# Kernel tuning notes

Measured on AMD Instinct MI355X. Metric: run time of the kernel, lower is better.

## Reference

```python
import jax, jax.numpy as jnp
import numpy as np

N_NODES = 50000
N_EDGES = 500000
F_DIM = 128
N_REL = 8
N_LAYERS = 2
NEG_SLOPE = 0.2  # PyG RGATConv default negative_slope


def setup_inputs() -> dict:
    key = jax.random.key(0)
    ks = jax.random.split(key, 6)
    x = jax.random.normal(ks[0], (N_NODES, F_DIM), dtype=jnp.float32)
    edge_index = jax.random.randint(ks[1], (2, N_EDGES), 0, N_NODES)
    edge_type = jax.random.randint(ks[2], (N_EDGES,), 0, N_REL)
    # Per-layer relation weights [L, R, F_in, F_out], attention vectors q,k [L, F_out, 1], bias [L, F_out]
    W = jax.random.normal(ks[3], (N_LAYERS, N_REL, F_DIM, F_DIM), dtype=jnp.float32) * (1.0 / np.sqrt(F_DIM)).astype(np.float32)
    att_q = jax.random.normal(ks[4], (N_LAYERS, F_DIM, 1), dtype=jnp.float32) * 0.1
    att_k = jax.random.normal(ks[5], (N_LAYERS, F_DIM, 1), dtype=jnp.float32) * 0.1
    bias = jnp.zeros((N_LAYERS, F_DIM), dtype=jnp.float32)
    return {"x": x, "W": W, "att_q": att_q, "att_k": att_k, "bias": bias,
            "edge_index": edge_index, "edge_type": edge_type}


def _segment_softmax(logits, seg, num_segments):
    # Numerically stable softmax over edges grouped by destination node.
    m = jax.ops.segment_max(logits, seg, num_segments=num_segments)
    m = jax.lax.stop_gradient(m)
    e = jnp.exp(logits - m[seg])
    denom = jax.ops.segment_sum(e, seg, num_segments=num_segments)
    return e / (denom[seg] + 1e-16)


def _rgat_layer(h, src, dst, edge_type, W, q, k, b):
    # h: [N, F]; W: [R, F, F]. Project once per relation, then gather per edge
    # (avoids materializing [E, F, F] per-edge weight gathers).
    n = h.shape[0]
    xw = jnp.einsum('nf,rfg->rng', h, W)          # [R, N, F]
    out_j = xw[edge_type, src]                    # [E, F] transformed source feats
    out_i = xw[edge_type, dst]                    # [E, F] transformed dest feats
    # additive self-attention: leaky_relu(q(x_i) + k(x_j)), heads=1, dim=1
    logits = jax.nn.leaky_relu((out_i @ q + out_j @ k)[:, 0], NEG_SLOPE)  # [E]
    alpha = _segment_softmax(logits, dst, n)      # across-relation softmax per dst node
    agg = jax.ops.segment_sum(alpha[:, None] * out_j, dst, num_segments=n)  # [N, F]
    return agg + b


def reference(x, W, att_q, att_k, bias, edge_index, edge_type):
    src, dst = edge_index[0], edge_index[1]
    h = x
    for l in range(W.shape[0]):  # small fixed layer count
        h = _rgat_layer(h, src, dst, edge_type, W[l], att_q[l], att_k[l], bias[l])
        h = jax.nn.relu(h)  # dropout is identity in eval mode
    return h
```

## Files before the change

kernel.cpp:

```cpp
#include <hip/hip_runtime.h>
#include <hip/hip_bf16.h>
#include <hip/hip_fp16.h>

#define N_NODES 50000
#define N_EDGES 500000
#define F_DIM   128
#define N_REL   8
#define N_LAYERS 2
#define NEG_SLOPE 0.2f

#define NBLK_N ((N_NODES + 255) / 256)

typedef _Float16 half8 __attribute__((ext_vector_type(8)));
typedef float f32x4  __attribute__((ext_vector_type(4)));


__device__ inline float lrelu(float l) { return (l > 0.f) ? l : NEG_SLOPE * l; }

__global__ __launch_bounds__(256) void prep_h(const float* __restrict__ H,
                                              _Float16* __restrict__ Hf) {
    const size_t i8 = (size_t)blockIdx.x * 256 + threadIdx.x;
    if (i8 >= (size_t)N_NODES * F_DIM / 8) return;
    const float* src = H + i8 * 8;
    float av[8];
    *(float4*)(av)     = *(const float4*)(src);
    *(float4*)(av + 4) = *(const float4*)(src + 4);
    alignas(16) _Float16 hb[8];
#pragma unroll
    for (int j = 0; j < 8; ++j) hb[j] = (_Float16)av[j];
    *(uint4*)(Hf + i8 * 8) = *(const uint4*)hb;
}

__global__ __launch_bounds__(256) void prep_w(const float* __restrict__ W,
                                              _Float16* __restrict__ Wf) {
    __shared__ float tile[64][F_DIM + 1];
    const int mat = blockIdx.x;
    const float* src = W + (size_t)mat * F_DIM * F_DIM;
    const int t = threadIdx.x;
    for (int hf = 0; hf < 2; ++hf) {
#pragma unroll
        for (int i = 0; i < 8; ++i) {
            int idx = t + i * 256;
            int f = idx >> 5, c4 = idx & 31;
            float4 v = *(const float4*)(src + (size_t)(hf * 64 + f) * F_DIM + c4 * 4);
            *(float4*)&tile[f][c4 * 4] = v;
        }
        __syncthreads();
        int g = t >> 1, fs = (t & 1) * 32;
        for (int c = 0; c < 4; ++c) {
            alignas(16) _Float16 th[8];
#pragma unroll
            for (int j = 0; j < 8; ++j) th[j] = (_Float16)tile[fs + c * 8 + j][g];
            size_t o = ((size_t)mat * F_DIM + g) * F_DIM + hf * 64 + fs + c * 8;
            *(uint4*)(Wf + o) = *(const uint4*)th;
        }
        __syncthreads();
    }
}

#define GBM 128
__global__ __launch_bounds__(256, 2) void gemm_xw(const _Float16* __restrict__ Hf,
                                                  const _Float16* __restrict__ Wf,
                                                  const float* __restrict__ qv_g,
                                                  const float* __restrict__ kv_g,
                                                  __half* __restrict__ xw,
                                                  float* __restrict__ a_q,
                                                  float* __restrict__ a_k) {
    __shared__ _Float16 lds[F_DIM * F_DIM];
    const int rb0 = blockIdx.x * GBM;
    const int r   = blockIdx.y;
    const int tid = threadIdx.x;
    const int lane = tid & 63, w = tid >> 6;
    const int q = lane >> 4, ln = lane & 15;

    {
        const _Float16* src = Wf + (size_t)r * F_DIM * F_DIM;
#pragma unroll
        for (int i = 0; i < 8; ++i) {
            int chunk = tid + i * 256;
            int gg = chunk >> 4, c8 = chunk & 15;
            uint4 v = *(const uint4*)(src + gg * F_DIM + c8 * 8);
            *(uint4*)(lds + gg * F_DIM + ((c8 ^ (gg & 15)) * 8)) = v;
        }
    }

    half8 Af[2][4];
#pragma unroll
    for (int rt = 0; rt < 2; ++rt) {
        int row = rb0 + w * 32 + rt * 16 + ln;
        int ar = (row < N_NODES) ? row : (N_NODES - 1);
        const _Float16* hp = Hf + (size_t)ar * F_DIM;
#pragma unroll
        for (int ks = 0; ks < 4; ++ks)
            Af[rt][ks] = *(const half8*)(hp + ks * 32 + q * 8);
    }

    float qvl[8], kvl[8];
#pragma unroll
    for (int t = 0; t < 8; ++t) {
        qvl[t] = qv_g[t * 16 + ln];
        kvl[t] = kv_g[t * 16 + ln];
    }

    __syncthreads();

    f32x4 acc[2][8];
#pragma unroll
    for (int rt = 0; rt < 2; ++rt)
#pragma unroll
        for (int t = 0; t < 8; ++t) acc[rt][t] = (f32x4)(0.f);

#pragma unroll
    for (int ks = 0; ks < 4; ++ks) {
        const int jx = (((ks * 4 + q) ^ ln)) << 3;
        half8 Bf[8];
#pragma unroll
        for (int c = 0; c < 8; ++c)
            Bf[c] = *(const half8*)(lds + (c * 16 + ln) * F_DIM + jx);
#pragma unroll
        for (int c = 0; c < 8; ++c)
#pragma unroll
            for (int rt = 0; rt < 2; ++rt)
                acc[rt][c] = __builtin_amdgcn_mfma_f32_16x16x32_f16(Af[rt][ks], Bf[c], acc[rt][c], 0, 0, 0);
    }

#pragma unroll
    for (int rt = 0; rt < 2; ++rt) {
        float pq[4], pk[4];
#pragma unroll
        for (int reg = 0; reg < 4; ++reg) {
            const int row = rb0 + w * 32 + rt * 16 + q * 4 + reg;
            alignas(16) unsigned short hs[8];
            float sq = 0.f, sk = 0.f;
#pragma unroll
            for (int t = 0; t < 8; ++t) {
                float v = acc[rt][t][reg];
                __half hv = __float2half(v);
                hs[t] = *reinterpret_cast<unsigned short*>(&hv);
                sq = fmaf(v, qvl[t], sq);
                sk = fmaf(v, kvl[t], sk);
            }
            if (row < N_NODES)
                *(uint4*)(xw + ((size_t)r * N_NODES + row) * F_DIM + ln * 8) = *(const uint4*)hs;
            pq[reg] = sq; pk[reg] = sk;
        }
#pragma unroll
        for (int reg = 0; reg < 4; ++reg) {
#pragma unroll
            for (int m = 1; m <= 8; m <<= 1) {
                pq[reg] += __shfl_xor(pq[reg], m);
                pk[reg] += __shfl_xor(pk[reg], m);
            }
        }
        if (ln == 0) {
#pragma unroll
            for (int reg = 0; reg < 4; ++reg) {
                const int row = rb0 + w * 32 + rt * 16 + q * 4 + reg;
                if (row < N_NODES) {
                    a_q[r * N_NODES + row] = pq[reg];
                    a_k[r * N_NODES + row] = pk[reg];
                }
            }
        }
    }
}


__global__ __launch_bounds__(256) void count_kernel(const int* __restrict__ dstp,
                                                    int* __restrict__ cnt) {
    int e = blockIdx.x * 256 + threadIdx.x;
    if (e < N_EDGES) atomicAdd(cnt + dstp[e], 1);
}

__global__ __launch_bounds__(256) void block_sum_kernel(const int* __restrict__ cnt,
                                                        int* __restrict__ partial) {
    __shared__ int s[256];
    int idx = blockIdx.x * 256 + threadIdx.x;
    int v = (idx < N_NODES) ? cnt[idx] : 0;
    s[threadIdx.x] = v;
    __syncthreads();
    for (int off = 128; off > 0; off >>= 1) {
        if (threadIdx.x < off) s[threadIdx.x] += s[threadIdx.x + off];
        __syncthreads();
    }
    if (threadIdx.x == 0) partial[blockIdx.x] = s[0];
}

__global__ __launch_bounds__(256) void scan_partials_kernel(int* __restrict__ partial,
                                                            int* __restrict__ row_ptr) {
    __shared__ int s[256];
    int t = threadIdx.x;
    int v = (t < NBLK_N) ? partial[t] : 0;
    s[t] = v;
    __syncthreads();
#pragma unroll
    for (int off = 1; off < 256; off <<= 1) {
        int x = (t >= off) ? s[t - off] : 0;
        __syncthreads();
        s[t] += x;
        __syncthreads();
    }
    if (t < NBLK_N) partial[t] = s[t] - v;
    if (t == 0) row_ptr[N_NODES] = N_EDGES;
}

__global__ __launch_bounds__(256) void scan_block_kernel(const int* __restrict__ cnt,
                                                         const int* __restrict__ partial,
                                                         int* __restrict__ row_ptr) {
    __shared__ int s[256];
    int t = threadIdx.x;
    int idx = blockIdx.x * 256 + t;
    int v = (idx < N_NODES) ? cnt[idx] : 0;
    s[t] = v;
    __syncthreads();
#pragma unroll
    for (int off = 1; off < 256; off <<= 1) {
        int x = (t >= off) ? s[t - off] : 0;
        __syncthreads();
        s[t] += x;
        __syncthreads();
    }
    if (idx < N_NODES) row_ptr[idx] = partial[blockIdx.x] + s[t] - v;
}

__global__ __launch_bounds__(256) void scatter_kernel(const int* __restrict__ srcp,
                                                      const int* __restrict__ dstp,
                                                      const int* __restrict__ etp,
                                                      const int* __restrict__ row_ptr,
                                                      int* __restrict__ cursor,
                                                      unsigned* __restrict__ sorted,
                                                      unsigned short* __restrict__ dst16) {
    int e = blockIdx.x * 256 + threadIdx.x;
    if (e >= N_EDGES) return;
    int d = dstp[e];
    int pos = atomicAdd(cursor + d, 1);
    int j = row_ptr[d] + pos;
    sorted[j] = (unsigned)srcp[e] | ((unsigned)etp[e] << 16);
    dst16[j] = (unsigned short)d;
}

__global__ __launch_bounds__(256) void logits_kernel(const float* __restrict__ a_q,
                                                     const float* __restrict__ a_k,
                                                     const unsigned* __restrict__ sorted,
                                                     const unsigned short* __restrict__ dst16,
                                                     float* __restrict__ lgt) {
    int j = blockIdx.x * 256 + threadIdx.x;
    if (j >= N_EDGES) return;
    unsigned p = sorted[j];
    int s = p & 0xffff, t = p >> 16;
    int d = dst16[j];
    lgt[j] = lrelu(a_q[t * N_NODES + d] + a_k[t * N_NODES + s]);
}

__device__ inline void accum8(float* acc, uint4 v, float a) {
    const __half2* h2 = reinterpret_cast<const __half2*>(&v);
#pragma unroll
    for (int t = 0; t < 4; ++t) {
        float2 f = __half22float2(h2[t]);
        acc[t * 2]     = fmaf(a, f.x, acc[t * 2]);
        acc[t * 2 + 1] = fmaf(a, f.y, acc[t * 2 + 1]);
    }
}
__device__ inline const uint4* xwrow(const __half* xw, unsigned p, int ln) {
    return (const uint4*)(xw + (((size_t)(p >> 16)) * N_NODES + (p & 0xffff)) * F_DIM + ln * 8);
}

__global__ __launch_bounds__(256) void agg_fused(const __half* __restrict__ xw,
                                                 const float* __restrict__ lgt,
                                                 const int* __restrict__ row_ptr,
                                                 const unsigned* __restrict__ sorted,
                                                 const float* __restrict__ bias,
                                                 float* __restrict__ outp,
                                                 _Float16* __restrict__ hfp) {
    const int lane = threadIdx.x & 63;
    const int wave = threadIdx.x >> 6;
    const int d = blockIdx.x * 4 + wave;
    if (d >= N_NODES) return;
    const int beg = row_ptr[d], end = row_ptr[d + 1];
    const int cnt = end - beg;
    const int g = lane >> 4, ln = lane & 15;

    if (cnt <= 64) {
        unsigned p = 0;
        float l = -3.4e38f;
        if (lane < cnt) {
            p = sorted[beg + lane];
            l = lgt[beg + lane];
        }
        float m = l;
#pragma unroll
        for (int off = 32; off > 0; off >>= 1) m = fmaxf(m, __shfl_xor(m, off));
        const float ex = (lane < cnt) ? __expf(l - m) : 0.f;

        float acc[8] = {0, 0, 0, 0, 0, 0, 0, 0};
        for (int i = 0; i < cnt; i += 8) {
            unsigned p0 = __shfl(p, i + g);
            unsigned p1 = __shfl(p, i + 4 + g);
            float a0 = __shfl(ex, i + g);
            float a1 = __shfl(ex, i + 4 + g);
            uint4 v0 = *xwrow(xw, p0, ln);
            uint4 v1 = *xwrow(xw, p1, ln);
            accum8(acc, v0, a0);
            accum8(acc, v1, a1);
        }
        float dsum = ex;
#pragma unroll
        for (int off = 32; off > 0; off >>= 1) dsum += __shfl_xor(dsum, off);
#pragma unroll
        for (int t = 0; t < 8; ++t) {
            acc[t] += __shfl_xor(acc[t], 16);
            acc[t] += __shfl_xor(acc[t], 32);
        }
        if (g == 0) {
            const float inv = 1.f / (dsum + 1e-16f);
#pragma unroll
            for (int t = 0; t < 8; ++t) {
                const int col = t * 16 + ln;
                const float v = fmaxf(fmaf(acc[t], inv, bias[col]), 0.f);
                if (outp) outp[(size_t)d * F_DIM + col] = v;
                if (hfp)  hfp[(size_t)d * F_DIM + col] = (_Float16)v;
            }
        }
    } else {
        const int p0 = lane * 2;
        const int c0 = (p0 & 7) * 16 + (p0 >> 3);
        const int c1 = c0 + 16;
        float2 acc = make_float2(bias[c0], bias[c1]);
        float m = -3.4e38f;
        for (int i = beg + lane; i < end; i += 64) m = fmaxf(m, lgt[i]);
#pragma unroll
        for (int off = 32; off > 0; off >>= 1) m = fmaxf(m, __shfl_xor(m, off));
        float dsum = 0.f;
        for (int i = beg + lane; i < end; i += 64) dsum += __expf(lgt[i] - m);
#pragma unroll
        for (int off = 32; off > 0; off >>= 1) dsum += __shfl_xor(dsum, off);
        const float inv = 1.f / (dsum + 1e-16f);
        for (int i = beg; i < end; ++i) {
            unsigned p = sorted[i];
            float alpha = __expf(lgt[i] - m) * inv;
            const __half2 h2 = *((const __half2*)xw + (((size_t)(p >> 16)) * N_NODES + (p & 0xffff)) * (F_DIM / 2) + lane);
            float2 v = make_float2(__half2float(h2.x), __half2float(h2.y));
            acc.x = fmaf(alpha, v.x, acc.x);
            acc.y = fmaf(alpha, v.y, acc.y);
        }
        const float v0 = fmaxf(acc.x, 0.f), v1 = fmaxf(acc.y, 0.f);
        if (outp) { outp[(size_t)d * F_DIM + c0] = v0; outp[(size_t)d * F_DIM + c1] = v1; }
        if (hfp)  { hfp[(size_t)d * F_DIM + c0] = (_Float16)v0; hfp[(size_t)d * F_DIM + c1] = (_Float16)v1; }
    }
}


extern "C" void kernel_launch(void* const* d_in, const int* in_sizes, int n_in,
                              void* d_out, int out_size, void* d_ws, size_t ws_size,
                              hipStream_t stream) {
    const float* x     = (const float*)d_in[0];
    const float* W     = (const float*)d_in[1];
    const float* att_q = (const float*)d_in[2];
    const float* att_k = (const float*)d_in[3];
    const float* bias  = (const float*)d_in[4];
    const int* ei      = (const int*)d_in[5];
    const int* etp     = (const int*)d_in[6];
    const int* srcp = ei;
    const int* dstp = ei + N_EDGES;
    float* out = (float*)d_out;
    char* ws   = (char*)d_ws;

    size_t off = 0;
    auto alloc = [&](size_t bytes) {
        void* p = ws + off;
        off = (off + bytes + 511) & ~(size_t)511;
        return p;
    };
    __half* xw       = (__half*)alloc((size_t)N_REL * N_NODES * F_DIM * sizeof(__half));
    float* a_q       = (float*)alloc((size_t)N_REL * N_NODES * sizeof(float));
    float* a_k       = (float*)alloc((size_t)N_REL * N_NODES * sizeof(float));
    int* cnt         = (int*)alloc((size_t)2 * N_NODES * sizeof(int));
    int* cursor      = cnt + N_NODES;
    int* row_ptr     = (int*)alloc(((size_t)N_NODES + 1) * sizeof(int));
    int* partial     = (int*)alloc(256 * sizeof(int));
    unsigned* sorted = (unsigned*)alloc((size_t)N_EDGES * sizeof(unsigned));
    unsigned short* dst16 = (unsigned short*)alloc((size_t)N_EDGES * sizeof(unsigned short));
    float* lgt       = (float*)alloc((size_t)N_EDGES * sizeof(float));
    _Float16* Wf     = (_Float16*)alloc((size_t)N_LAYERS * N_REL * F_DIM * F_DIM * sizeof(_Float16));
    _Float16* Hf     = (_Float16*)alloc((size_t)N_NODES * F_DIM * sizeof(_Float16));

    prep_w<<<N_LAYERS * N_REL, 256, 0, stream>>>(W, Wf);
    hipMemsetAsync(cnt, 0, (size_t)2 * N_NODES * 4, stream);
    count_kernel<<<(N_EDGES + 255) / 256, 256, 0, stream>>>(dstp, cnt);
    block_sum_kernel<<<NBLK_N, 256, 0, stream>>>(cnt, partial);
    scan_partials_kernel<<<1, 256, 0, stream>>>(partial, row_ptr);
    scan_block_kernel<<<NBLK_N, 256, 0, stream>>>(cnt, partial, row_ptr);
    scatter_kernel<<<(N_EDGES + 255) / 256, 256, 0, stream>>>(
        srcp, dstp, etp, row_ptr, cursor, sorted, dst16);

    const int grid_h = (N_NODES * F_DIM / 8 + 255) / 256;
    const int grid_m = (N_NODES + GBM - 1) / GBM;
    const int grid_e = (N_EDGES + 255) / 256;
    prep_h<<<grid_h, 256, 0, stream>>>(x, Hf);
    for (int l = 0; l < N_LAYERS; ++l) {
        gemm_xw<<<dim3(grid_m, N_REL), 256, 0, stream>>>(
            Hf, Wf + (size_t)l * N_REL * F_DIM * F_DIM,
            att_q + l * F_DIM, att_k + l * F_DIM,
            xw, a_q, a_k);
        logits_kernel<<<grid_e, 256, 0, stream>>>(a_q, a_k, sorted, dst16, lgt);
        const bool last = (l == N_LAYERS - 1);
        agg_fused<<<(N_NODES + 3) / 4, 256, 0, stream>>>(
            xw, lgt, row_ptr, sorted, bias + l * F_DIM,
            last ? out : nullptr,
            last ? nullptr : Hf);
    }
}
```

Baseline: 301.5 us.

## Aggregate raw features per relation then project, folding attention into W·q vectors

Instead of materializing the per-relation projection xw for all nodes (R×N×F fp16), the attention scalars are computed directly from H times precomputed W·q and W·k vectors. Edges are sorted by (dst, relation), raw source features are aggregated per relation, and then multiplied by W_r with MFMA inside the aggregation kernel. This removes the large xw write and read traffic and the dense R-fold GEMM, in exchange for a more complex aggregation kernel with per-relation synchronisation, extra CSR preprocessing, and fp16 rounding of aggregated sums.

Measured after the change: 571.1 us. +89.4%, slower.

```diff
diff --git a/kernel.cpp b/kernel.cpp
--- a/kernel.cpp
+++ b/kernel.cpp
@@ -16,6 +16,16 @@
 
 
 __device__ inline float lrelu(float l) { return (l > 0.f) ? l : NEG_SLOPE * l; }
+
+__device__ inline void accum8h(float* a, uint4 v, float al) {
+    const __half2* h2 = reinterpret_cast<const __half2*>(&v);
+#pragma unroll
+    for (int t = 0; t < 4; ++t) {
+        float2 f = __half22float2(h2[t]);
+        a[t * 2]     = fmaf(al, f.x, a[t * 2]);
+        a[t * 2 + 1] = fmaf(al, f.y, a[t * 2 + 1]);
+    }
+}
 
 __global__ __launch_bounds__(256) void prep_h(const float* __restrict__ H,
                                               _Float16* __restrict__ Hf) {
@@ -58,118 +68,67 @@
     }
 }
 
-#define GBM 128
-__global__ __launch_bounds__(256, 2) void gemm_xw(const _Float16* __restrict__ Hf,
-                                                  const _Float16* __restrict__ Wf,
-                                                  const float* __restrict__ qv_g,
-                                                  const float* __restrict__ kv_g,
-                                                  __half* __restrict__ xw,
+__global__ __launch_bounds__(256) void prep_vqk(const float* __restrict__ W,
+                                                const float* __restrict__ att_q,
+                                                const float* __restrict__ att_k,
+                                                _Float16* __restrict__ vb) {
+    const int l = blockIdx.x >> 3, r = blockIdx.x & 7;
+    __shared__ float qk[2 * F_DIM];
+    const int t = threadIdx.x;
+    qk[t] = (t < F_DIM) ? att_q[l * F_DIM + t] : att_k[l * F_DIM + (t - F_DIM)];
+    __syncthreads();
+    const float* Wr = W + ((size_t)(l * N_REL + r)) * F_DIM * F_DIM;
+    const int f = t & (F_DIM - 1);
+    const float* qv = (t < F_DIM) ? qk : qk + F_DIM;
+    float s = 0.f;
+    for (int g = 0; g < F_DIM; g += 4) {
+        float4 wv = *(const float4*)(Wr + (size_t)f * F_DIM + g);
+        s += wv.x * qv[g] + wv.y * qv[g + 1] + wv.z * qv[g + 2] + wv.w * qv[g + 3];
+    }
+    const int c = (t < F_DIM) ? r : (N_REL + r);
+    vb[((size_t)l * 16 + c) * F_DIM + f] = (_Float16)s;
+}
+
+__global__ __launch_bounds__(256) void aqk_kernel(const _Float16* __restrict__ Hf,
+                                                  const _Float16* __restrict__ vbl,
                                                   float* __restrict__ a_q,
                                                   float* __restrict__ a_k) {
-    __shared__ _Float16 lds[F_DIM * F_DIM];
-    const int rb0 = blockIdx.x * GBM;
-    const int r   = blockIdx.y;
-    const int tid = threadIdx.x;
-    const int lane = tid & 63, w = tid >> 6;
+    const int w = threadIdx.x >> 6, lane = threadIdx.x & 63;
     const int q = lane >> 4, ln = lane & 15;
-
-    {
-        const _Float16* src = Wf + (size_t)r * F_DIM * F_DIM;
-#pragma unroll
-        for (int i = 0; i < 8; ++i) {
-            int chunk = tid + i * 256;
-            int gg = chunk >> 4, c8 = chunk & 15;
-            uint4 v = *(const uint4*)(src + gg * F_DIM + c8 * 8);
-            *(uint4*)(lds + gg * F_DIM + ((c8 ^ (gg & 15)) * 8)) = v;
-        }
-    }
-
-    half8 Af[2][4];
-#pragma unroll
-    for (int rt = 0; rt < 2; ++rt) {
-        int row = rb0 + w * 32 + rt * 16 + ln;
-        int ar = (row < N_NODES) ? row : (N_NODES - 1);
-        const _Float16* hp = Hf + (size_t)ar * F_DIM;
-#pragma unroll
-        for (int ks = 0; ks < 4; ++ks)
-            Af[rt][ks] = *(const half8*)(hp + ks * 32 + q * 8);
-    }
-
-    float qvl[8], kvl[8];
-#pragma unroll
-    for (int t = 0; t < 8; ++t) {
-        qvl[t] = qv_g[t * 16 + ln];
-        kvl[t] = kv_g[t * 16 + ln];
-    }
-
-    __syncthreads();
-
-    f32x4 acc[2][8];
-#pragma unroll
-    for (int rt = 0; rt < 2; ++rt)
-#pragma unroll
-        for (int t = 0; t < 8; ++t) acc[rt][t] = (f32x4)(0.f);
-
+    const int row0 = blockIdx.x * 64 + w * 16;
+    f32x4 acc = (f32x4)(0.f);
 #pragma unroll
     for (int ks = 0; ks < 4; ++ks) {
-        const int jx = (((ks * 4 + q) ^ ln)) << 3;
-        half8 Bf[8];
-#pragma unroll
-        for (int c = 0; c < 8; ++c)
-            Bf[c] = *(const half8*)(lds + (c * 16 + ln) * F_DIM + jx);
-#pragma unroll
-        for (int c = 0; c < 8; ++c)
-#pragma unroll
-            for (int rt = 0; rt < 2; ++rt)
-                acc[rt][c] = __builtin_amdgcn_mfma_f32_16x16x32_f16(Af[rt][ks], Bf[c], acc[rt][c], 0, 0, 0);
-    }
-
-#pragma unroll
-    for (int rt = 0; rt < 2; ++rt) {
-        float pq[4], pk[4];
-#pragma unroll
-        for (int reg = 0; reg < 4; ++reg) {
-            const int row = rb0 + w * 32 + rt * 16 + q * 4 + reg;
-            alignas(16) unsigned short hs[8];
-            float sq = 0.f, sk = 0.f;
-#pragma unroll
-            for (int t = 0; t < 8; ++t) {
-                float v = acc[rt][t][reg];
-                __half hv = __float2half(v);
-                hs[t] = *reinterpret_cast<unsigned short*>(&hv);
-                sq = fmaf(v, qvl[t], sq);
-                sk = fmaf(v, kvl[t], sk);
-            }
-            if (row < N_NODES)
-                *(uint4*)(xw + ((size_t)r * N_NODES + row) * F_DIM + ln * 8) = *(const uint4*)hs;
-            pq[reg] = sq; pk[reg] = sk;
-        }
-#pragma unroll
-        for (int reg = 0; reg < 4; ++reg) {
-#pragma unroll
-            for (int m = 1; m <= 8; m <<= 1) {
-                pq[reg] += __shfl_xor(pq[reg], m);
-                pk[reg] += __shfl_xor(pk[reg], m);
-            }
-        }
-        if (ln == 0) {
-#pragma unroll
-            for (int reg = 0; reg < 4; ++reg) {
-                const int row = rb0 + w * 32 + rt * 16 + q * 4 + reg;
-                if (row < N_NODES) {
-                    a_q[r * N_NODES + row] = pq[reg];
-                    a_k[r * N_NODES + row] = pk[reg];
-                }
-            }
-        }
-    }
-}
-
-
-__global__ __launch_bounds__(256) void count_kernel(const int* __restrict__ dstp,
-                                                    int* __restrict__ cnt) {
+        int rr = row0 + ln; if (rr >= N_NODES) rr = N_NODES - 1;
+        half8 af = *(const half8*)(Hf + (size_t)rr * F_DIM + ks * 32 + q * 8);
+        half8 bf = *(const half8*)(vbl + (size_t)ln * F_DIM + ks * 32 + q * 8);
+        acc = __builtin_amdgcn_mfma_f32_16x16x32_f16(af, bf, acc, 0, 0, 0);
+    }
+#pragma unroll
+    for (int reg = 0; reg < 4; ++reg) {
+        const int row = row0 + q * 4 + reg;
+        if (row < N_NODES) {
+            if (ln < N_REL) a_q[ln * N_NODES + row] = acc[reg];
+            else            a_k[(ln - N_REL) * N_NODES + row] = acc[reg];
+        }
+    }
+}
+
+
+__global__ __launch_bounds__(256) void count2_kernel(const int* __restrict__ dstp,
+                                                     const int* __restrict__ etp,
+                                                     int* __restrict__ cnt2) {
     int e = blockIdx.x * 256 + threadIdx.x;
-    if (e < N_EDGES) atomicAdd(cnt + dstp[e], 1);
+    if (e < N_EDGES) atomicAdd(cnt2 + dstp[e] * N_REL + etp[e], 1);
+}
+
+__global__ __launch_bounds__(256) void sum8_kernel(const int* __restrict__ cnt2,
+                                                   int* __restrict__ cnt) {
+    int d = blockIdx.x * 256 + threadIdx.x;
+    if (d >= N_NODES) return;
+    int4 a = *(const int4*)(cnt2 + d * 8);
+    int4 b = *(const int4*)(cnt2 + d * 8 + 4);
+    cnt[d] = a.x + a.y + a.z + a.w + b.x + b.y + b.z + b.w;
 }
 
 __global__ __launch_bounds__(256) void block_sum_kernel(const int* __restrict__ cnt,
@@ -223,19 +182,35 @@
     if (idx < N_NODES) row_ptr[idx] = partial[blockIdx.x] + s[t] - v;
 }
 
-__global__ __launch_bounds__(256) void scatter_kernel(const int* __restrict__ srcp,
-                                                      const int* __restrict__ dstp,
-                                                      const int* __restrict__ etp,
-                                                      const int* __restrict__ row_ptr,
-                                                      int* __restrict__ cursor,
-                                                      unsigned* __restrict__ sorted,
-                                                      unsigned short* __restrict__ dst16) {
+__global__ __launch_bounds__(256) void rp2_kernel(const int* __restrict__ cnt2,
+                                                  const int* __restrict__ row_ptr,
+                                                  int* __restrict__ rp2) {
+    int d = blockIdx.x * 256 + threadIdx.x;
+    if (d == 0) rp2[(size_t)N_NODES * 8] = N_EDGES;
+    if (d >= N_NODES) return;
+    int4 a = *(const int4*)(cnt2 + d * 8);
+    int4 b = *(const int4*)(cnt2 + d * 8 + 4);
+    int rp = row_ptr[d];
+    int o[8];
+    o[0] = rp;          o[1] = o[0] + a.x;  o[2] = o[1] + a.y;  o[3] = o[2] + a.z;
+    o[4] = o[3] + a.w;  o[5] = o[4] + b.x;  o[6] = o[5] + b.y;  o[7] = o[6] + b.z;
+    *(int4*)(rp2 + d * 8)     = make_int4(o[0], o[1], o[2], o[3]);
+    *(int4*)(rp2 + d * 8 + 4) = make_int4(o[4], o[5], o[6], o[7]);
+}
+
+__global__ __launch_bounds__(256) void scatter2_kernel(const int* __restrict__ srcp,
+                                                       const int* __restrict__ dstp,
+                                                       const int* __restrict__ etp,
+                                                       const int* __restrict__ rp2,
+                                                       int* __restrict__ cursor2,
+                                                       unsigned* __restrict__ sorted,
+                                                       unsigned short* __restrict__ dst16) {
     int e = blockIdx.x * 256 + threadIdx.x;
     if (e >= N_EDGES) return;
-    int d = dstp[e];
-    int pos = atomicAdd(cursor + d, 1);
-    int j = row_ptr[d] + pos;
-    sorted[j] = (unsigned)srcp[e] | ((unsigned)etp[e] << 16);
+    int d = dstp[e], r = etp[e];
+    int pos = atomicAdd(cursor2 + d * N_REL + r, 1);
+    int j = rp2[d * N_REL + r] + pos;
+    sorted[j] = (unsigned)srcp[e] | ((unsigned)r << 16);
     dst16[j] = (unsigned short)d;
 }
 
@@ -252,101 +227,180 @@
     lgt[j] = lrelu(a_q[t * N_NODES + d] + a_k[t * N_NODES + s]);
 }
 
-__device__ inline void accum8(float* acc, uint4 v, float a) {
-    const __half2* h2 = reinterpret_cast<const __half2*>(&v);
-#pragma unroll
-    for (int t = 0; t < 4; ++t) {
-        float2 f = __half22float2(h2[t]);
-        acc[t * 2]     = fmaf(a, f.x, acc[t * 2]);
-        acc[t * 2 + 1] = fmaf(a, f.y, acc[t * 2 + 1]);
-    }
-}
-__device__ inline const uint4* xwrow(const __half* xw, unsigned p, int ln) {
-    return (const uint4*)(xw + (((size_t)(p >> 16)) * N_NODES + (p & 0xffff)) * F_DIM + ln * 8);
-}
-
-__global__ __launch_bounds__(256) void agg_fused(const __half* __restrict__ xw,
-                                                 const float* __restrict__ lgt,
-                                                 const int* __restrict__ row_ptr,
-                                                 const unsigned* __restrict__ sorted,
-                                                 const float* __restrict__ bias,
-                                                 float* __restrict__ outp,
-                                                 _Float16* __restrict__ hfp) {
-    const int lane = threadIdx.x & 63;
-    const int wave = threadIdx.x >> 6;
-    const int d = blockIdx.x * 4 + wave;
-    if (d >= N_NODES) return;
-    const int beg = row_ptr[d], end = row_ptr[d + 1];
-    const int cnt = end - beg;
+__global__ __launch_bounds__(256) void agg_mfma(const _Float16* __restrict__ Hf,
+                                                const _Float16* __restrict__ Wf,
+                                                const float* __restrict__ lgt,
+                                                const unsigned* __restrict__ sorted,
+                                                const int* __restrict__ rp2,
+                                                const float* __restrict__ bias,
+                                                float* __restrict__ outp,
+                                                _Float16* __restrict__ hfp) {
+    __shared__ float S[32][F_DIM];
+    __shared__ float sm[32], sinv[32];
+    const int tid = threadIdx.x, lane = tid & 63, w = tid >> 6;
     const int g = lane >> 4, ln = lane & 15;
-
-    if (cnt <= 64) {
-        unsigned p = 0;
-        float l = -3.4e38f;
-        if (lane < cnt) {
-            p = sorted[beg + lane];
-            l = lgt[beg + lane];
-        }
-        float m = l;
-#pragma unroll
-        for (int off = 32; off > 0; off >>= 1) m = fmaxf(m, __shfl_xor(m, off));
-        const float ex = (lane < cnt) ? __expf(l - m) : 0.f;
-
-        float acc[8] = {0, 0, 0, 0, 0, 0, 0, 0};
-        for (int i = 0; i < cnt; i += 8) {
-            unsigned p0 = __shfl(p, i + g);
-            unsigned p1 = __shfl(p, i + 4 + g);
-            float a0 = __shfl(ex, i + g);
-            float a1 = __shfl(ex, i + 4 + g);
-            uint4 v0 = *xwrow(xw, p0, ln);
-            uint4 v1 = *xwrow(xw, p1, ln);
-            accum8(acc, v0, a0);
-            accum8(acc, v1, a1);
-        }
-        float dsum = ex;
-#pragma unroll
-        for (int off = 32; off > 0; off >>= 1) dsum += __shfl_xor(dsum, off);
-#pragma unroll
-        for (int t = 0; t < 8; ++t) {
-            acc[t] += __shfl_xor(acc[t], 16);
-            acc[t] += __shfl_xor(acc[t], 32);
-        }
-        if (g == 0) {
-            const float inv = 1.f / (dsum + 1e-16f);
+    const int q = g;
+    const int base = blockIdx.x * 32;
+
+    int rpv[8];
+    unsigned pc[8];
+    float lc[8], ex[8];
+    int beg_[8], deg_[8];
+    const int lidx = (lane <= 8) ? lane : 8;
+#pragma unroll
+    for (int i = 0; i < 8; ++i) {
+        int d = base + w * 8 + i;
+        int dd = (d < N_NODES) ? d : (N_NODES - 1);
+        rpv[i] = rp2[dd * 8 + lidx];
+    }
+#pragma unroll
+    for (int i = 0; i < 8; ++i) {
+        int b = __shfl(rpv[i], 0);
+        int e = __shfl(rpv[i], 8);
+        beg_[i] = b; deg_[i] = e - b;
+        if (deg_[i] <= 64) {
+            pc[i] = (lane < deg_[i]) ? sorted[b + lane] : 0u;
+            lc[i] = (lane < deg_[i]) ? lgt[b + lane] : -3.4e38f;
+        } else { pc[i] = 0u; lc[i] = -3.4e38f; }
+    }
+#pragma unroll
+    for (int i = 0; i < 8; ++i) {
+        if (deg_[i] <= 64) {
+            float m = lc[i];
+#pragma unroll
+            for (int off = 32; off > 0; off >>= 1) m = fmaxf(m, __shfl_xor(m, off));
+            float e0 = (lane < deg_[i]) ? __expf(lc[i] - m) : 0.f;
+            ex[i] = e0;
+            float ds = e0;
+#pragma unroll
+            for (int off = 32; off > 0; off >>= 1) ds += __shfl_xor(ds, off);
+            if (lane == 0) { sm[w * 8 + i] = m; sinv[w * 8 + i] = 1.f / (ds + 1e-16f); }
+        } else {
+            ex[i] = 0.f;
+            const int b = beg_[i], e = b + deg_[i];
+            float m = -3.4e38f;
+            for (int j = b + lane; j < e; j += 64) m = fmaxf(m, lgt[j]);
+#pragma unroll
+            for (int off = 32; off > 0; off >>= 1) m = fmaxf(m, __shfl_xor(m, off));
+            float ds = 0.f;
+            for (int j = b + lane; j < e; j += 64) ds += __expf(lgt[j] - m);
+#pragma unroll
+            for (int off = 32; off > 0; off >>= 1) ds += __shfl_xor(ds, off);
+            if (lane == 0) { sm[w * 8 + i] = m; sinv[w * 8 + i] = 1.f / (ds + 1e-16f); }
+        }
+    }
+    __syncthreads();
+
+    f32x4 acc[2][2];
+#pragma unroll
+    for (int rt = 0; rt < 2; ++rt)
+#pragma unroll
+        for (int ct = 0; ct < 2; ++ct) acc[rt][ct] = (f32x4)(0.f);
+
+#pragma unroll 1
+    for (int r = 0; r < N_REL; ++r) {
+#pragma unroll
+        for (int i = 0; i < 8; ++i) {
+            const int sr = __shfl(rpv[i], r);
+            const int er = __shfl(rpv[i], r + 1);
+            const int cr = er - sr;
+            const int row = w * 8 + i;
+            if (cr == 0) {
+                if (g == 0) {
+                    float4* dp = (float4*)&S[row][(ln ^ (row & 15)) << 3];
+                    dp[0] = make_float4(0.f, 0.f, 0.f, 0.f);
+                    dp[1] = make_float4(0.f, 0.f, 0.f, 0.f);
+                }
+                continue;
+            }
+            float a8[8] = {0, 0, 0, 0, 0, 0, 0, 0};
+            if (deg_[i] <= 64) {
+                const int o = sr - beg_[i];
+                for (int jj = 0; jj < cr; jj += 8) {
+                    int j0 = (o + jj + g) & 63;
+                    int j1 = (o + jj + 4 + g) & 63;
+                    unsigned p0 = __shfl(pc[i], j0);
+                    unsigned p1 = __shfl(pc[i], j1);
+                    float a0 = __shfl(ex[i], j0);
+                    float a1 = __shfl(ex[i], j1);
+                    if (jj + g >= cr) a0 = 0.f;
+                    if (jj + 4 + g >= cr) a1 = 0.f;
+                    uint4 v0 = *(const uint4*)(Hf + (size_t)(p0 & 0xffff) * F_DIM + ln * 8);
+                    uint4 v1 = *(const uint4*)(Hf + (size_t)(p1 & 0xffff) * F_DIM + ln * 8);
+                    accum8h(a8, v0, a0);
+                    accum8h(a8, v1, a1);
+                }
+            } else {
+                const float mi = sm[row];
+                for (int j = sr; j < er; j += 8) {
+                    int i0 = j + g, i1 = j + 4 + g;
+                    unsigned p0 = 0, p1 = 0;
+                    float a0 = 0.f, a1 = 0.f;
+                    if (i0 < er) { p0 = sorted[i0]; a0 = __expf(lgt[i0] - mi); }
+                    if (i1 < er) { p1 = sorted[i1]; a1 = __expf(lgt[i1] - mi); }
+                    uint4 v0 = *(const uint4*)(Hf + (size_t)(p0 & 0xffff) * F_DIM + ln * 8);
+                    uint4 v1 = *(const uint4*)(Hf + (size_t)(p1 & 0xffff) * F_DIM + ln * 8);
+                    accum8h(a8, v0, a0);
+                    accum8h(a8, v1, a1);
+                }
+            }
 #pragma unroll
             for (int t = 0; t < 8; ++t) {
-                const int col = t * 16 + ln;
-                const float v = fmaxf(fmaf(acc[t], inv, bias[col]), 0.f);
-                if (outp) outp[(size_t)d * F_DIM + col] = v;
-                if (hfp)  hfp[(size_t)d * F_DIM + col] = (_Float16)v;
-            }
-        }
-    } else {
-        const int p0 = lane * 2;
-        const int c0 = (p0 & 7) * 16 + (p0 >> 3);
-        const int c1 = c0 + 16;
-        float2 acc = make_float2(bias[c0], bias[c1]);
-        float m = -3.4e38f;
-        for (int i = beg + lane; i < end; i += 64) m = fmaxf(m, lgt[i]);
-#pragma unroll
-        for (int off = 32; off > 0; off >>= 1) m = fmaxf(m, __shfl_xor(m, off));
-        float dsum = 0.f;
-        for (int i = beg + lane; i < end; i += 64) dsum += __expf(lgt[i] - m);
-#pragma unroll
-        for (int off = 32; off > 0; off >>= 1) dsum += __shfl_xor(dsum, off);
-        const float inv = 1.f / (dsum + 1e-16f);
-        for (int i = beg; i < end; ++i) {
-            unsigned p = sorted[i];
-            float alpha = __expf(lgt[i] - m) * inv;
-            const __half2 h2 = *((const __half2*)xw + (((size_t)(p >> 16)) * N_NODES + (p & 0xffff)) * (F_DIM / 2) + lane);
-            float2 v = make_float2(__half2float(h2.x), __half2float(h2.y));
-            acc.x = fmaf(alpha, v.x, acc.x);
-            acc.y = fmaf(alpha, v.y, acc.y);
-        }
-        const float v0 = fmaxf(acc.x, 0.f), v1 = fmaxf(acc.y, 0.f);
-        if (outp) { outp[(size_t)d * F_DIM + c0] = v0; outp[(size_t)d * F_DIM + c1] = v1; }
-        if (hfp)  { hfp[(size_t)d * F_DIM + c0] = (_Float16)v0; hfp[(size_t)d * F_DIM + c1] = (_Float16)v1; }
-    }
+                a8[t] += __shfl_xor(a8[t], 16);
+                a8[t] += __shfl_xor(a8[t], 32);
+            }
+            if (g == 0) {
+                float4* dp = (float4*)&S[row][(ln ^ (row & 15)) << 3];
+                dp[0] = make_float4(a8[0], a8[1], a8[2], a8[3]);
+                dp[1] = make_float4(a8[4], a8[5], a8[6], a8[7]);
+            }
+        }
+        __syncthreads();
+
+        const _Float16* Wfr = Wf + (size_t)r * F_DIM * F_DIM;
+#pragma unroll
+        for (int ks = 0; ks < 4; ++ks) {
+            half8 af[2];
+#pragma unroll
+            for (int rt = 0; rt < 2; ++rt) {
+                const float* sp = &S[rt * 16 + ln][((ks * 4 + q) ^ ln) << 3];
+                float4 f0 = *(const float4*)sp;
+                float4 f1 = *((const float4*)sp + 1);
+                af[rt][0] = (_Float16)f0.x; af[rt][1] = (_Float16)f0.y;
+                af[rt][2] = (_Float16)f0.z; af[rt][3] = (_Float16)f0.w;
+                af[rt][4] = (_Float16)f1.x; af[rt][5] = (_Float16)f1.y;
+                af[rt][6] = (_Float16)f1.z; af[rt][7] = (_Float16)f1.w;
+            }
+            half8 bf[2];
+#pragma unroll
+            for (int ct = 0; ct < 2; ++ct)
+                bf[ct] = *(const half8*)(Wfr + (size_t)((w * 2 + ct) * 16 + ln) * F_DIM + ks * 32 + q * 8);
+#pragma unroll
+            for (int rt = 0; rt < 2; ++rt)
+#pragma unroll
+                for (int ct = 0; ct < 2; ++ct)
+                    acc[rt][ct] = __builtin_amdgcn_mfma_f32_16x16x32_f16(af[rt], bf[ct], acc[rt][ct], 0, 0, 0);
+        }
+        __syncthreads();
+    }
+
+#pragma unroll
+    for (int rt = 0; rt < 2; ++rt)
+#pragma unroll
+        for (int ct = 0; ct < 2; ++ct) {
+            const int col = (w * 2 + ct) * 16 + ln;
+            const float bs = bias[col];
+#pragma unroll
+            for (int reg = 0; reg < 4; ++reg) {
+                const int row = rt * 16 + q * 4 + reg;
+                const int d = base + row;
+                if (d < N_NODES) {
+                    const float v = fmaxf(fmaf(acc[rt][ct][reg], sinv[row], bs), 0.f);
+                    if (outp) outp[(size_t)d * F_DIM + col] = v;
+                    if (hfp)  hfp[(size_t)d * F_DIM + col] = (_Float16)v;
+                }
+            }
+        }
 }
 
 
@@ -371,42 +425,48 @@
         off = (off + bytes + 511) & ~(size_t)511;
         return p;
     };
-    __half* xw       = (__half*)alloc((size_t)N_REL * N_NODES * F_DIM * sizeof(__half));
+    _Float16* Hf0    = (_Float16*)alloc((size_t)N_NODES * F_DIM * sizeof(_Float16));
+    _Float16* Hf1    = (_Float16*)alloc((size_t)N_NODES * F_DIM * sizeof(_Float16));
+    _Float16* Wf     = (_Float16*)alloc((size_t)N_LAYERS * N_REL * F_DIM * F_DIM * sizeof(_Float16));
+    _Float16* vb     = (_Float16*)alloc((size_t)N_LAYERS * 16 * F_DIM * sizeof(_Float16));
     float* a_q       = (float*)alloc((size_t)N_REL * N_NODES * sizeof(float));
     float* a_k       = (float*)alloc((size_t)N_REL * N_NODES * sizeof(float));
-    int* cnt         = (int*)alloc((size_t)2 * N_NODES * sizeof(int));
-    int* cursor      = cnt + N_NODES;
+    int* cnt2        = (int*)alloc((size_t)2 * N_NODES * N_REL * sizeof(int));
+    int* cursor2     = cnt2 + (size_t)N_NODES * N_REL;
+    int* cnt         = (int*)alloc((size_t)N_NODES * sizeof(int));
     int* row_ptr     = (int*)alloc(((size_t)N_NODES + 1) * sizeof(int));
     int* partial     = (int*)alloc(256 * sizeof(int));
+    int* rp2         = (int*)alloc(((size_t)N_NODES * N_REL + 1) * sizeof(int));
     unsigned* sorted = (unsigned*)alloc((size_t)N_EDGES * sizeof(unsigned));
     unsigned short* dst16 = (unsigned short*)alloc((size_t)N_EDGES * sizeof(unsigned short));
     float* lgt       = (float*)alloc((size_t)N_EDGES * sizeof(float));
-    _Float16* Wf     = (_Float16*)alloc((size_t)N_LAYERS * N_REL * F_DIM * F_DIM * sizeof(_Float16));
-    _Float16* Hf     = (_Float16*)alloc((size_t)N_NODES * F_DIM * sizeof(_Float16));
 
     prep_w<<<N_LAYERS * N_REL, 256, 0, stream>>>(W, Wf);
-    hipMemsetAsync(cnt, 0, (size_t)2 * N_NODES * 4, stream);
-    count_kernel<<<(N_EDGES + 255) / 256, 256, 0, stream>>>(dstp, cnt);
+    prep_vqk<<<N_LAYERS * N_REL, 256, 0, stream>>>(W, att_q, att_k, vb);
+    hipMemsetAsync(cnt2, 0, (size_t)2 * N_NODES * N_REL * sizeof(int), stream);
+    count2_kernel<<<(N_EDGES + 255) / 256, 256, 0, stream>>>(dstp, etp, cnt2);
+    sum8_kernel<<<NBLK_N, 256, 0, stream>>>(cnt2, cnt);
     block_sum_kernel<<<NBLK_N, 256, 0, stream>>>(cnt, partial);
     scan_partials_kernel<<<1, 256, 0, stream>>>(partial, row_ptr);
     scan_block_kernel<<<NBLK_N, 256, 0, stream>>>(cnt, partial, row_ptr);
-    scatter_kernel<<<(N_EDGES + 255) / 256, 256, 0, stream>>>(
-        srcp, dstp, etp, row_ptr, cursor, sorted, dst16);
+    rp2_kernel<<<NBLK_N, 256, 0, stream>>>(cnt2, row_ptr, rp2);
+    scatter2_kernel<<<(N_EDGES + 255) / 256, 256, 0, stream>>>(
+        srcp, dstp, etp, rp2, cursor2, sorted, dst16);
 
     const int grid_h = (N_NODES * F_DIM / 8 + 255) / 256;
-    const int grid_m = (N_NODES + GBM - 1) / GBM;
     const int grid_e = (N_EDGES + 255) / 256;
-    prep_h<<<grid_h, 256, 0, stream>>>(x, Hf);
+    const int grid_a = (N_NODES + 63) / 64;
+    const int grid_f = (N_NODES + 31) / 32;
+    prep_h<<<grid_h, 256, 0, stream>>>(x, Hf0);
     for (int l = 0; l < N_LAYERS; ++l) {
-        gemm_xw<<<dim3(grid_m, N_REL), 256, 0, stream>>>(
-            Hf, Wf + (size_t)l * N_REL * F_DIM * F_DIM,
-            att_q + l * F_DIM, att_k + l * F_DIM,
-            xw, a_q, a_k);
+        const _Float16* Hin = (l == 0) ? Hf0 : Hf1;
+        const bool last = (l == N_LAYERS - 1);
+        aqk_kernel<<<grid_a, 256, 0, stream>>>(Hin, vb + (size_t)l * 16 * F_DIM, a_q, a_k);
         logits_kernel<<<grid_e, 256, 0, stream>>>(a_q, a_k, sorted, dst16, lgt);
-        const bool last = (l == N_LAYERS - 1);
-        agg_fused<<<(N_NODES + 3) / 4, 256, 0, stream>>>(
-            xw, lgt, row_ptr, sorted, bias + l * F_DIM,
+        agg_mfma<<<grid_f, 256, 0, stream>>>(
+            Hin, Wf + (size_t)l * N_REL * F_DIM * F_DIM, lgt, sorted, rp2,
+            bias + l * F_DIM,
             last ? out : nullptr,
-            last ? nullptr : Hf);
-    }
-}
+            last ? nullptr : Hf1);
+    }
+}
```

## Split aggregation waves across two nodes and loop GEMM over four row tiles

Applied to the files above, without the earlier changes.

The aggregation kernel now gives each 32-lane half-wave its own destination node, with half-width shuffles when both nodes have at most 32 edges. When either node has more, it falls back to full-wave processing of each node in turn. This targets the many idle lanes left by low average in-degree. Separately, each GEMM block now covers four 128-row tiles and reuses the relation weight loaded once into LDS, cutting repeated W loads at the cost of fewer blocks in the grid.

Result: faster. 291.6 us (-3.3%).

```diff
diff --git a/kernel.cpp b/kernel.cpp
--- a/kernel.cpp
+++ b/kernel.cpp
@@ -58,7 +58,7 @@
     }
 }
 
-#define GBM 128
+#define GBM 512
 __global__ __launch_bounds__(256, 2) void gemm_xw(const _Float16* __restrict__ Hf,
                                                   const _Float16* __restrict__ Wf,
                                                   const float* __restrict__ qv_g,
@@ -67,7 +67,6 @@
                                                   float* __restrict__ a_q,
                                                   float* __restrict__ a_k) {
     __shared__ _Float16 lds[F_DIM * F_DIM];
-    const int rb0 = blockIdx.x * GBM;
     const int r   = blockIdx.y;
     const int tid = threadIdx.x;
     const int lane = tid & 63, w = tid >> 6;
@@ -84,17 +83,6 @@
         }
     }
 
-    half8 Af[2][4];
-#pragma unroll
-    for (int rt = 0; rt < 2; ++rt) {
-        int row = rb0 + w * 32 + rt * 16 + ln;
-        int ar = (row < N_NODES) ? row : (N_NODES - 1);
-        const _Float16* hp = Hf + (size_t)ar * F_DIM;
-#pragma unroll
-        for (int ks = 0; ks < 4; ++ks)
-            Af[rt][ks] = *(const half8*)(hp + ks * 32 + q * 8);
-    }
-
     float qvl[8], kvl[8];
 #pragma unroll
     for (int t = 0; t < 8; ++t) {
@@ -104,61 +92,77 @@
 
     __syncthreads();
 
-    f32x4 acc[2][8];
-#pragma unroll
-    for (int rt = 0; rt < 2; ++rt)
-#pragma unroll
-        for (int t = 0; t < 8; ++t) acc[rt][t] = (f32x4)(0.f);
-
-#pragma unroll
-    for (int ks = 0; ks < 4; ++ks) {
-        const int jx = (((ks * 4 + q) ^ ln)) << 3;
-        half8 Bf[8];
-#pragma unroll
-        for (int c = 0; c < 8; ++c)
-            Bf[c] = *(const half8*)(lds + (c * 16 + ln) * F_DIM + jx);
-#pragma unroll
-        for (int c = 0; c < 8; ++c)
-#pragma unroll
-            for (int rt = 0; rt < 2; ++rt)
-                acc[rt][c] = __builtin_amdgcn_mfma_f32_16x16x32_f16(Af[rt][ks], Bf[c], acc[rt][c], 0, 0, 0);
-    }
-
-#pragma unroll
-    for (int rt = 0; rt < 2; ++rt) {
-        float pq[4], pk[4];
-#pragma unroll
-        for (int reg = 0; reg < 4; ++reg) {
-            const int row = rb0 + w * 32 + rt * 16 + q * 4 + reg;
-            alignas(16) unsigned short hs[8];
-            float sq = 0.f, sk = 0.f;
-#pragma unroll
-            for (int t = 0; t < 8; ++t) {
-                float v = acc[rt][t][reg];
-                __half hv = __float2half(v);
-                hs[t] = *reinterpret_cast<unsigned short*>(&hv);
-                sq = fmaf(v, qvl[t], sq);
-                sk = fmaf(v, kvl[t], sk);
-            }
-            if (row < N_NODES)
-                *(uint4*)(xw + ((size_t)r * N_NODES + row) * F_DIM + ln * 8) = *(const uint4*)hs;
-            pq[reg] = sq; pk[reg] = sk;
-        }
-#pragma unroll
-        for (int reg = 0; reg < 4; ++reg) {
-#pragma unroll
-            for (int m = 1; m <= 8; m <<= 1) {
-                pq[reg] += __shfl_xor(pq[reg], m);
-                pk[reg] += __shfl_xor(pk[reg], m);
-            }
-        }
-        if (ln == 0) {
+    for (int t4 = 0; t4 < 4; ++t4) {
+        const int rb0 = blockIdx.x * GBM + t4 * 128;
+        if (rb0 >= N_NODES) break;
+
+        half8 Af[2][4];
+#pragma unroll
+        for (int rt = 0; rt < 2; ++rt) {
+            int row = rb0 + w * 32 + rt * 16 + ln;
+            int ar = (row < N_NODES) ? row : (N_NODES - 1);
+            const _Float16* hp = Hf + (size_t)ar * F_DIM;
+#pragma unroll
+            for (int ks = 0; ks < 4; ++ks)
+                Af[rt][ks] = *(const half8*)(hp + ks * 32 + q * 8);
+        }
+
+        f32x4 acc[2][8];
+#pragma unroll
+        for (int rt = 0; rt < 2; ++rt)
+#pragma unroll
+            for (int t = 0; t < 8; ++t) acc[rt][t] = (f32x4)(0.f);
+
+#pragma unroll
+        for (int ks = 0; ks < 4; ++ks) {
+            const int jx = (((ks * 4 + q) ^ ln)) << 3;
+            half8 Bf[8];
+#pragma unroll
+            for (int c = 0; c < 8; ++c)
+                Bf[c] = *(const half8*)(lds + (c * 16 + ln) * F_DIM + jx);
+#pragma unroll
+            for (int c = 0; c < 8; ++c)
+#pragma unroll
+                for (int rt = 0; rt < 2; ++rt)
+                    acc[rt][c] = __builtin_amdgcn_mfma_f32_16x16x32_f16(Af[rt][ks], Bf[c], acc[rt][c], 0, 0, 0);
+        }
+
+#pragma unroll
+        for (int rt = 0; rt < 2; ++rt) {
+            float pq[4], pk[4];
 #pragma unroll
             for (int reg = 0; reg < 4; ++reg) {
                 const int row = rb0 + w * 32 + rt * 16 + q * 4 + reg;
-                if (row < N_NODES) {
-                    a_q[r * N_NODES + row] = pq[reg];
-                    a_k[r * N_NODES + row] = pk[reg];
+                alignas(16) unsigned short hs[8];
+                float sq = 0.f, sk = 0.f;
+#pragma unroll
+                for (int t = 0; t < 8; ++t) {
+                    float v = acc[rt][t][reg];
+                    __half hv = __float2half(v);
+                    hs[t] = *reinterpret_cast<unsigned short*>(&hv);
+                    sq = fmaf(v, qvl[t], sq);
+                    sk = fmaf(v, kvl[t], sk);
+                }
+                if (row < N_NODES)
+                    *(uint4*)(xw + ((size_t)r * N_NODES + row) * F_DIM + ln * 8) = *(const uint4*)hs;
+                pq[reg] = sq; pk[reg] = sk;
+            }
+#pragma unroll
+            for (int reg = 0; reg < 4; ++reg) {
+#pragma unroll
+                for (int m = 1; m <= 8; m <<= 1) {
+                    pq[reg] += __shfl_xor(pq[reg], m);
+                    pk[reg] += __shfl_xor(pk[reg], m);
+                }
+            }
+            if (ln == 0) {
+#pragma unroll
+                for (int reg = 0; reg < 4; ++reg) {
+                    const int row = rb0 + w * 32 + rt * 16 + q * 4 + reg;
+                    if (row < N_NODES) {
+                        a_q[r * N_NODES + row] = pq[reg];
+                        a_k[r * N_NODES + row] = pk[reg];
+                    }
                 }
             }
         }
@@ -274,30 +278,35 @@
                                                  _Float16* __restrict__ hfp) {
     const int lane = threadIdx.x & 63;
     const int wave = threadIdx.x >> 6;
-    const int d = blockIdx.x * 4 + wave;
-    if (d >= N_NODES) return;
-    const int beg = row_ptr[d], end = row_ptr[d + 1];
-    const int cnt = end - beg;
-    const int g = lane >> 4, ln = lane & 15;
-
-    if (cnt <= 64) {
+    const int half = lane >> 5, hl = lane & 31;
+    const int d0 = blockIdx.x * 8 + wave * 2;
+    if (d0 >= N_NODES) return;
+    const int dmy = d0 + half;
+    const int dv = (dmy < N_NODES) ? dmy : (N_NODES - 1);
+    const int beg = row_ptr[dv], end = row_ptr[dv + 1];
+    int cnt = (dmy < N_NODES) ? (end - beg) : 0;
+    const int cntO = __shfl_xor(cnt, 32);
+    const int cmax = (cnt > cntO) ? cnt : cntO;
+
+    if (cmax <= 32) {
         unsigned p = 0;
         float l = -3.4e38f;
-        if (lane < cnt) {
-            p = sorted[beg + lane];
-            l = lgt[beg + lane];
+        if (hl < cnt) {
+            p = sorted[beg + hl];
+            l = lgt[beg + hl];
         }
         float m = l;
 #pragma unroll
-        for (int off = 32; off > 0; off >>= 1) m = fmaxf(m, __shfl_xor(m, off));
-        const float ex = (lane < cnt) ? __expf(l - m) : 0.f;
-
+        for (int off = 16; off > 0; off >>= 1) m = fmaxf(m, __shfl_xor(m, off, 32));
+        const float ex = (hl < cnt) ? __expf(l - m) : 0.f;
+
+        const int gg = hl >> 4, ln = hl & 15;
         float acc[8] = {0, 0, 0, 0, 0, 0, 0, 0};
-        for (int i = 0; i < cnt; i += 8) {
-            unsigned p0 = __shfl(p, i + g);
-            unsigned p1 = __shfl(p, i + 4 + g);
-            float a0 = __shfl(ex, i + g);
-            float a1 = __shfl(ex, i + 4 + g);
+        for (int i = 0; i < cnt; i += 4) {
+            unsigned p0 = __shfl(p, i + gg, 32);
+            unsigned p1 = __shfl(p, i + 2 + gg, 32);
+            float a0 = __shfl(ex, i + gg, 32);
+            float a1 = __shfl(ex, i + 2 + gg, 32);
             uint4 v0 = *xwrow(xw, p0, ln);
             uint4 v1 = *xwrow(xw, p1, ln);
             accum8(acc, v0, a0);
@@ -305,47 +314,94 @@
         }
         float dsum = ex;
 #pragma unroll
-        for (int off = 32; off > 0; off >>= 1) dsum += __shfl_xor(dsum, off);
-#pragma unroll
-        for (int t = 0; t < 8; ++t) {
-            acc[t] += __shfl_xor(acc[t], 16);
-            acc[t] += __shfl_xor(acc[t], 32);
-        }
-        if (g == 0) {
+        for (int off = 16; off > 0; off >>= 1) dsum += __shfl_xor(dsum, off, 32);
+#pragma unroll
+        for (int t = 0; t < 8; ++t) acc[t] += __shfl_xor(acc[t], 16, 32);
+
+        if (dmy < N_NODES) {
             const float inv = 1.f / (dsum + 1e-16f);
 #pragma unroll
-            for (int t = 0; t < 8; ++t) {
+            for (int j = 0; j < 4; ++j) {
+                const int t = gg * 4 + j;
                 const int col = t * 16 + ln;
                 const float v = fmaxf(fmaf(acc[t], inv, bias[col]), 0.f);
-                if (outp) outp[(size_t)d * F_DIM + col] = v;
-                if (hfp)  hfp[(size_t)d * F_DIM + col] = (_Float16)v;
+                if (outp) outp[(size_t)dmy * F_DIM + col] = v;
+                if (hfp)  hfp[(size_t)dmy * F_DIM + col] = (_Float16)v;
             }
         }
     } else {
-        const int p0 = lane * 2;
-        const int c0 = (p0 & 7) * 16 + (p0 >> 3);
-        const int c1 = c0 + 16;
-        float2 acc = make_float2(bias[c0], bias[c1]);
-        float m = -3.4e38f;
-        for (int i = beg + lane; i < end; i += 64) m = fmaxf(m, lgt[i]);
-#pragma unroll
-        for (int off = 32; off > 0; off >>= 1) m = fmaxf(m, __shfl_xor(m, off));
-        float dsum = 0.f;
-        for (int i = beg + lane; i < end; i += 64) dsum += __expf(lgt[i] - m);
-#pragma unroll
-        for (int off = 32; off > 0; off >>= 1) dsum += __shfl_xor(dsum, off);
-        const float inv = 1.f / (dsum + 1e-16f);
-        for (int i = beg; i < end; ++i) {
-            unsigned p = sorted[i];
-            float alpha = __expf(lgt[i] - m) * inv;
-            const __half2 h2 = *((const __half2*)xw + (((size_t)(p >> 16)) * N_NODES + (p & 0xffff)) * (F_DIM / 2) + lane);
-            float2 v = make_float2(__half2float(h2.x), __half2float(h2.y));
-            acc.x = fmaf(alpha, v.x, acc.x);
-            acc.y = fmaf(alpha, v.y, acc.y);
-        }
-        const float v0 = fmaxf(acc.x, 0.f), v1 = fmaxf(acc.y, 0.f);
-        if (outp) { outp[(size_t)d * F_DIM + c0] = v0; outp[(size_t)d * F_DIM + c1] = v1; }
-        if (hfp)  { hfp[(size_t)d * F_DIM + c0] = (_Float16)v0; hfp[(size_t)d * F_DIM + c1] = (_Float16)v1; }
+        const int g = lane >> 4, ln = lane & 15;
+        for (int h = 0; h < 2; ++h) {
+            const int dd = d0 + h;
+            if (dd >= N_NODES) continue;
+            const int b = __shfl(beg, h * 32);
+            const int c = __shfl(cnt, h * 32);
+            if (c <= 64) {
+                unsigned p = 0;
+                float l = -3.4e38f;
+                if (lane < c) {
+                    p = sorted[b + lane];
+                    l = lgt[b + lane];
+                }
+                float m = l;
+#pragma unroll
+                for (int off = 32; off > 0; off >>= 1) m = fmaxf(m, __shfl_xor(m, off));
+                const float ex = (lane < c) ? __expf(l - m) : 0.f;
+                float acc[8] = {0, 0, 0, 0, 0, 0, 0, 0};
+                for (int i = 0; i < c; i += 8) {
+                    unsigned p0 = __shfl(p, i + g);
+                    unsigned p1 = __shfl(p, i + 4 + g);
+                    float a0 = __shfl(ex, i + g);
+                    float a1 = __shfl(ex, i + 4 + g);
+                    uint4 v0 = *xwrow(xw, p0, ln);
+                    uint4 v1 = *xwrow(xw, p1, ln);
+                    accum8(acc, v0, a0);
+                    accum8(acc, v1, a1);
+                }
+                float dsum = ex;
+#pragma unroll
+                for (int off = 32; off > 0; off >>= 1) dsum += __shfl_xor(dsum, off);
+#pragma unroll
+                for (int t = 0; t < 8; ++t) {
+                    acc[t] += __shfl_xor(acc[t], 16);
+                    acc[t] += __shfl_xor(acc[t], 32);
+                }
+                const float inv = 1.f / (dsum + 1e-16f);
+#pragma unroll
+                for (int j = 0; j < 2; ++j) {
+                    const int t = g * 2 + j;
+                    const int col = t * 16 + ln;
+                    const float v = fmaxf(fmaf(acc[t], inv, bias[col]), 0.f);
+                    if (outp) outp[(size_t)dd * F_DIM + col] = v;
+                    if (hfp)  hfp[(size_t)dd * F_DIM + col] = (_Float16)v;
+                }
+            } else {
+                const int p0 = lane * 2;
+                const int c0 = (p0 & 7) * 16 + (p0 >> 3);
+                const int c1 = c0 + 16;
+                float2 acc = make_float2(bias[c0], bias[c1]);
+                float m = -3.4e38f;
+                for (int i = b + lane; i < b + c; i += 64) m = fmaxf(m, lgt[i]);
+#pragma unroll
+                for (int off = 32; off > 0; off >>= 1) m = fmaxf(m, __shfl_xor(m, off));
+                float dsum = 0.f;
+                for (int i = b + lane; i < b + c; i += 64) dsum += __expf(lgt[i] - m);
+#pragma unroll
+                for (int off = 32; off > 0; off >>= 1) dsum += __shfl_xor(dsum, off);
+                const float inv = 1.f / (dsum + 1e-16f);
+                for (int i = b; i < b + c; ++i) {
+                    unsigned pp = sorted[i];
+                    float alpha = __expf(lgt[i] - m) * inv;
+                    const __half2 h2 = *((const __half2*)xw + (((size_t)(pp >> 16)) * N_NODES + (pp & 0xffff)) * (F_DIM / 2) + lane);
+                    float2 v = make_float2(__half2float(h2.x), __half2float(h2.y));
+                    acc.x = fmaf(alpha, v.x, acc.x);
+                    acc.y = fmaf(alpha, v.y, acc.y);
+                }
+                const float v0 = fmaxf(acc.x, 0.f), v1 = fmaxf(acc.y, 0.f);
+                if (outp) { outp[(size_t)dd * F_DIM + c0] = v0; outp[(size_t)dd * F_DIM + c1] = v1; }
+                if (hfp)  { hfp[(size_t)dd * F_DIM + c0] = (_Float16)v0; hfp[(size_t)dd * F_DIM + c1] = (_Float16)v1; }
+            }
+        }
     }
 }
 
@@ -404,7 +460,7 @@
             xw, a_q, a_k);
         logits_kernel<<<grid_e, 256, 0, stream>>>(a_q, a_k, sorted, dst16, lgt);
         const bool last = (l == N_LAYERS - 1);
-        agg_fused<<<(N_NODES + 3) / 4, 256, 0, stream>>>(
+        agg_fused<<<(N_NODES + 7) / 8, 256, 0, stream>>>(
             xw, lgt, row_ptr, sorted, bias + l * F_DIM,
             last ? out : nullptr,
             last ? nullptr : Hf);
```
